# Kernel tuning notes

Hardware: AMD Instinct MI355X
Metric: run time of the kernel (lower is better)

## Reference

```python
import jax, jax.numpy as jnp
import numpy as np

B, T, D_IN, H, L, D_OUT = 32, 512, 512, 1024, 2, 512


def _init(key, shape, fan_in):
    bound = 1.0 / np.sqrt(fan_in)
    return jax.random.uniform(key, shape, jnp.float32, -bound, bound)


def setup_inputs() -> dict:
    key = jax.random.key(0)
    ks = jax.random.split(key, 16)
    inp = {"x": jax.random.normal(ks[0], (B, T, D_IN), jnp.float32)}
    # layer 0: input D_IN -> H ; layer 1: input H -> H
    inp["W_ih0"] = _init(ks[1], (3 * H, D_IN), H)
    inp["W_hh0"] = _init(ks[2], (3 * H, H), H)
    inp["b_ih0"] = _init(ks[3], (3 * H,), H)
    inp["b_hh0"] = _init(ks[4], (3 * H,), H)
    inp["W_ih1"] = _init(ks[5], (3 * H, H), H)
    inp["W_hh1"] = _init(ks[6], (3 * H, H), H)
    inp["b_ih1"] = _init(ks[7], (3 * H,), H)
    inp["b_hh1"] = _init(ks[8], (3 * H,), H)
    inp["W_fc"] = _init(ks[9], (D_OUT, H), H)
    inp["b_fc"] = _init(ks[10], (D_OUT,), H)
    return inp


def _gru_layer(x_tbd, Wih, Whh, bih, bhh):
    """x_tbd: [T, B, D]. Returns output sequence [T, B, H].
    PyTorch GRUCell gating:
      r = sigmoid(xr + hr); z = sigmoid(xz + hz)
      n = tanh(xn + r * hn); h' = (1 - z) * n + z * h
    """
    # precompute input projections for all timesteps: [T, B, 3H]
    x_proj = jnp.einsum('tbd,gd->tbg', x_tbd, Wih) + bih
    h0 = jnp.zeros((x_tbd.shape[1], Whh.shape[1]), x_tbd.dtype)

    def step(h, xp):
        hp = h @ Whh.T + bhh  # [B, 3H]
        xr, xz, xn = jnp.split(xp, 3, axis=-1)
        hr, hz, hn = jnp.split(hp, 3, axis=-1)
        r = jax.nn.sigmoid(xr + hr)
        z = jax.nn.sigmoid(xz + hz)
        n = jnp.tanh(xn + r * hn)
        h_new = (1.0 - z) * n + z * h
        return h_new, h_new

    _, out_seq = jax.lax.scan(step, h0, x_proj)
    return out_seq  # [T, B, H]


def reference(x, W_ih0, W_hh0, b_ih0, b_hh0, W_ih1, W_hh1, b_ih1, b_hh1, W_fc, b_fc):
    x_tbd = jnp.transpose(x, (1, 0, 2))  # [T, B, D_IN]
    h1_seq = _gru_layer(x_tbd, W_ih0, W_hh0, b_ih0, b_hh0)   # [T, B, H]
    h2_seq = _gru_layer(h1_seq, W_ih1, W_hh1, b_ih1, b_hh1)  # [T, B, H]
    last = h2_seq[-1]  # outs[-1].squeeze() -> [B, H]
    return last @ W_fc.T + b_fc  # [B, D_OUT]
```

## Files before the change

kernel.cpp:

```cpp
#include <hip/hip_runtime.h>

typedef unsigned short ushort;
typedef __attribute__((ext_vector_type(8))) short short8;
typedef __attribute__((ext_vector_type(4))) float f32x4;
typedef __attribute__((ext_vector_type(4))) unsigned short us4;
typedef __attribute__((ext_vector_type(4))) unsigned int u32x4;

#define BB 32
#define TT 512
#define DIN 512
#define HH 1024
#define CHUNK 128
#define SENT 0xFFFFFFFFu

__device__ __forceinline__ ushort f2b(float f) {
  unsigned u = __builtin_bit_cast(unsigned, f);
  unsigned r = (u + 0x7fffu + ((u >> 16) & 1u)) >> 16;
  return (ushort)r;
}

#define MFMA16(a, b, c) __builtin_amdgcn_mfma_f32_16x16x32_bf16(a, b, c, 0, 0, 0)

__device__ __forceinline__ void AS(unsigned* p, unsigned v) {
  __hip_atomic_store(p, v, __ATOMIC_RELAXED, __HIP_MEMORY_SCOPE_AGENT);
}

__device__ __forceinline__ bool fok(const u32x4& v) {
  return v[0] != SENT && v[1] != SENT && v[2] != SENT && v[3] != SENT;
}

__device__ __forceinline__ void poll8(const ushort* b, short8* f) {
  u32x4 t0, t1, t2, t3, t4, t5, t6, t7;
  while (true) {
    asm volatile(
        "global_load_dwordx4 %0, %8, off sc0 sc1\n\t"
        "global_load_dwordx4 %1, %9, off sc0 sc1\n\t"
        "global_load_dwordx4 %2, %10, off sc0 sc1\n\t"
        "global_load_dwordx4 %3, %11, off sc0 sc1\n\t"
        "global_load_dwordx4 %4, %12, off sc0 sc1\n\t"
        "global_load_dwordx4 %5, %13, off sc0 sc1\n\t"
        "global_load_dwordx4 %6, %14, off sc0 sc1\n\t"
        "global_load_dwordx4 %7, %15, off sc0 sc1\n\t"
        "s_waitcnt vmcnt(0)"
        : "=&v"(t0), "=&v"(t1), "=&v"(t2), "=&v"(t3),
          "=&v"(t4), "=&v"(t5), "=&v"(t6), "=&v"(t7)
        : "v"(b), "v"(b + 32), "v"(b + 64), "v"(b + 96),
          "v"(b + 128), "v"(b + 160), "v"(b + 192), "v"(b + 224)
        : "memory");
    bool ok = fok(t0) && fok(t1) && fok(t2) && fok(t3) &&
              fok(t4) && fok(t5) && fok(t6) && fok(t7);
    if (__all((int)ok)) break;
    __builtin_amdgcn_s_sleep(1);
  }
  f[0] = __builtin_bit_cast(short8, t0); f[1] = __builtin_bit_cast(short8, t1);
  f[2] = __builtin_bit_cast(short8, t2); f[3] = __builtin_bit_cast(short8, t3);
  f[4] = __builtin_bit_cast(short8, t4); f[5] = __builtin_bit_cast(short8, t5);
  f[6] = __builtin_bit_cast(short8, t6); f[7] = __builtin_bit_cast(short8, t7);
}

__device__ __forceinline__ void poll4(const ushort* b, short8* f) {
  u32x4 t0, t1, t2, t3;
  while (true) {
    asm volatile(
        "global_load_dwordx4 %0, %4, off sc0 sc1\n\t"
        "global_load_dwordx4 %1, %5, off sc0 sc1\n\t"
        "global_load_dwordx4 %2, %6, off sc0 sc1\n\t"
        "global_load_dwordx4 %3, %7, off sc0 sc1\n\t"
        "s_waitcnt vmcnt(0)"
        : "=&v"(t0), "=&v"(t1), "=&v"(t2), "=&v"(t3)
        : "v"(b), "v"(b + 32), "v"(b + 64), "v"(b + 96)
        : "memory");
    bool ok = fok(t0) && fok(t1) && fok(t2) && fok(t3);
    if (__all((int)ok)) break;
    __builtin_amdgcn_s_sleep(1);
  }
  f[0] = __builtin_bit_cast(short8, t0); f[1] = __builtin_bit_cast(short8, t1);
  f[2] = __builtin_bit_cast(short8, t2); f[3] = __builtin_bit_cast(short8, t3);
}

__global__ __launch_bounds__(256) void init_k(unsigned int* h1s, unsigned int* h2s) {
  int i = blockIdx.x * 256 + threadIdx.x;
  if (i < 16384) h1s[i] = 0u;
  else h2s[i - 16384] = 0u;
}

__global__ __launch_bounds__(256) void refill_k(u32x4* a, u32x4* b) {
  size_t i = (size_t)blockIdx.x * 256 + threadIdx.x;
  u32x4 s = {SENT, SENT, SENT, SENT};
  a[i] = s;
  b[i] = s;
}

__global__ __launch_bounds__(256) void cast_k(const float* __restrict__ in,
                                              ushort* __restrict__ out, int n4) {
  int i = blockIdx.x * 256 + threadIdx.x;
  if (i < n4) {
    float4 v = ((const float4*)in)[i];
    us4 o;
    o.x = f2b(v.x); o.y = f2b(v.y); o.z = f2b(v.z); o.w = f2b(v.w);
    ((us4*)out)[i] = o;
  }
}

__global__ __launch_bounds__(256) void gemm_bt(const float* __restrict__ A32,
                                               const ushort* __restrict__ B,
                                               float* __restrict__ C,
                                               int N, int K, int tOff) {
  __shared__ __align__(16) ushort As[128 * 72];
  __shared__ __align__(16) ushort Bs[128 * 72];
  const int tid = threadIdx.x;
  const int lane = tid & 63, wave = tid >> 6;
  const int wm = wave >> 1, wn = wave & 1;
  const int bm = blockIdx.y << 7, bn = blockIdx.x << 7;

  const int srow = tid >> 3;
  const int sdst = (tid & 7) << 3;
  size_t aoff[4], boff[4];
#pragma unroll
  for (int i = 0; i < 4; ++i) {
    int m = bm + srow + (i << 5);
    aoff[i] = ((size_t)(m & 31) * TT + tOff + (m >> 5)) * (size_t)K;
    boff[i] = (size_t)(bn + srow + (i << 5)) * K;
  }

  const int fr = lane & 15, fq = lane >> 4;
  int aofl[4], bofl[4];
#pragma unroll
  for (int m = 0; m < 4; ++m) {
    aofl[m] = ((wm << 6) + (m << 4) + fr) * 72 + (fq << 3);
    bofl[m] = ((wn << 6) + (m << 4) + fr) * 72 + (fq << 3);
  }

  f32x4 acc[4][4] = {};
  for (int k0 = 0; k0 < K; k0 += 64) {
#pragma unroll
    for (int i = 0; i < 4; ++i) {
      int row = srow + (i << 5);
      float4 v0 = *(const float4*)&A32[aoff[i] + k0 + sdst];
      float4 v1 = *(const float4*)&A32[aoff[i] + k0 + sdst + 4];
      us4 lo, hi;
      lo.x = f2b(v0.x); lo.y = f2b(v0.y); lo.z = f2b(v0.z); lo.w = f2b(v0.w);
      hi.x = f2b(v1.x); hi.y = f2b(v1.y); hi.z = f2b(v1.z); hi.w = f2b(v1.w);
      *(us4*)&As[row * 72 + sdst] = lo;
      *(us4*)&As[row * 72 + sdst + 4] = hi;
      *(short8*)&Bs[row * 72 + sdst] = *(const short8*)&B[boff[i] + k0 + sdst];
    }
    __syncthreads();
#pragma unroll
    for (int kk = 0; kk < 2; ++kk) {
      short8 af[4], bf[4];
#pragma unroll
      for (int m = 0; m < 4; ++m) af[m] = *(const short8*)&As[aofl[m] + kk * 32];
#pragma unroll
      for (int n = 0; n < 4; ++n) bf[n] = *(const short8*)&Bs[bofl[n] + kk * 32];
#pragma unroll
      for (int m = 0; m < 4; ++m)
#pragma unroll
        for (int n = 0; n < 4; ++n)
          acc[m][n] = MFMA16(af[m], bf[n], acc[m][n]);
    }
    __syncthreads();
  }
#pragma unroll
  for (int m = 0; m < 4; ++m) {
    int row0 = bm + (wm << 6) + (m << 4) + (fq << 2);
#pragma unroll
    for (int n = 0; n < 4; ++n) {
      int col = bn + (wn << 6) + (n << 4) + fr;
#pragma unroll
      for (int r = 0; r < 4; ++r)
        C[(size_t)(row0 + r) * N + col] = acc[m][n][r];
    }
  }
}

__global__ __launch_bounds__(512, 1) void gru_fused(
    const ushort* __restrict__ wh0, const ushort* __restrict__ wh1,
    const ushort* __restrict__ wi1,
    const float* __restrict__ bih0, const float* __restrict__ bhh0,
    const float* __restrict__ bih1, const float* __restrict__ bhh1,
    const float* __restrict__ xp,
    ushort* __restrict__ h1, ushort* __restrict__ h2,
    float* __restrict__ hs0, float* __restrict__ hs1,
    int t0, int nSteps) {
  __shared__ float P[8][24][64];
  const int tid = threadIdx.x;
  const int wv = tid >> 6, lane = tid & 63;
  const int fr = lane & 15, fq = lane >> 4;
  const int layer = blockIdx.x >> 6;
  const int c0 = (blockIdx.x & 63) << 4;
  const int c = c0 + fr;
  const int cpair = c0 + (fr & ~1);

  if (layer == 0) {
    const int K0 = wv << 7;
    short8 wf[3][4];
#pragma unroll
    for (int g = 0; g < 3; ++g)
#pragma unroll
      for (int j = 0; j < 4; ++j)
        wf[g][j] = *(const short8*)&wh0[(size_t)(g * HH + c) * HH + K0 + j * 32 + fq * 8];

    float bhr = 0, bhz = 0, bhn = 0, bir = 0, biz = 0, bin_ = 0;
    float hl[4] = {};
    if (wv < 2) {
      bhr = bhh0[c]; bhz = bhh0[HH + c]; bhn = bhh0[2 * HH + c];
      bir = bih0[c]; biz = bih0[HH + c]; bin_ = bih0[2 * HH + c];
      if (t0 > 0)
#pragma unroll
        for (int r = 0; r < 4; ++r) hl[r] = hs0[(wv * 16 + (fq << 2) + r) * HH + c];
    }

    for (int i = 0; i < nSteps; ++i) {
      float xr[4], xz[4], xn[4];
      if (wv < 2) {
        const float* xpt = xp + (size_t)i * (BB * 3 * HH);
#pragma unroll
        for (int r = 0; r < 4; ++r) {
          const float* p = xpt + (size_t)(wv * 16 + (fq << 2) + r) * (3 * HH) + c;
          xr[r] = p[0]; xz[r] = p[HH]; xn[r] = p[2 * HH];
        }
      }
      const ushort* sb = h1 + (size_t)i * (BB * HH);
      short8 a0[4], a1[4];
      poll4(sb + fr * HH + K0 + fq * 8, a0);
      poll4(sb + (fr + 16) * HH + K0 + fq * 8, a1);
      f32x4 acc[2][3] = {};
#pragma unroll
      for (int j = 0; j < 4; ++j) {
        acc[0][0] = MFMA16(a0[j], wf[0][j], acc[0][0]);
        acc[0][1] = MFMA16(a0[j], wf[1][j], acc[0][1]);
        acc[0][2] = MFMA16(a0[j], wf[2][j], acc[0][2]);
        acc[1][0] = MFMA16(a1[j], wf[0][j], acc[1][0]);
        acc[1][1] = MFMA16(a1[j], wf[1][j], acc[1][1]);
        acc[1][2] = MFMA16(a1[j], wf[2][j], acc[1][2]);
      }
#pragma unroll
      for (int mt = 0; mt < 2; ++mt)
#pragma unroll
        for (int g = 0; g < 3; ++g)
#pragma unroll
          for (int r = 0; r < 4; ++r)
            P[wv][mt * 12 + g * 4 + r][lane] = acc[mt][g][r];
      __syncthreads();

      if (wv < 2) {
        float s[3][4];
#pragma unroll
        for (int g = 0; g < 3; ++g)
#pragma unroll
          for (int r = 0; r < 4; ++r) {
            int e = wv * 12 + g * 4 + r;
            float v = 0.f;
#pragma unroll
            for (int w = 0; w < 8; ++w) v += P[w][e][lane];
            s[g][r] = v;
          }
        ushort* hw = h1 + (size_t)(i + 1) * (BB * HH);
        const bool last = (i == nSteps - 1);
#pragma unroll
        for (int r = 0; r < 4; ++r) {
          float rv = 1.f / (1.f + __expf(-(xr[r] + bir + s[0][r] + bhr)));
          float zv = 1.f / (1.f + __expf(-(xz[r] + biz + s[1][r] + bhz)));
          float nv = tanhf(xn[r] + bin_ + rv * (s[2][r] + bhn));
          float h = (1.f - zv) * nv + zv * hl[r];
          hl[r] = h;
          unsigned me = f2b(h);
          unsigned nb = (unsigned)__shfl_xor((int)me, 1);
          unsigned word = me | (nb << 16);
          int b = wv * 16 + (fq << 2) + r;
          if ((lane & 1) == 0)
            AS((unsigned*)(hw + (size_t)b * HH + cpair), word);
          if (last) {
            hs0[b * HH + c] = h;
            if ((lane & 1) == 0)
              *(unsigned*)(h1 + (size_t)b * HH + cpair) = word;
          }
        }
      }
      __syncthreads();
    }
  } else {
    const int K0 = (wv & 3) << 8;
    const ushort* Wm = (wv < 4) ? wh1 : wi1;
    short8 wf[3][8];
#pragma unroll
    for (int g = 0; g < 3; ++g)
#pragma unroll
      for (int j = 0; j < 8; ++j)
        wf[g][j] = *(const short8*)&Wm[(size_t)(g * HH + c) * HH + K0 + j * 32 + fq * 8];

    float bhr = 0, bhz = 0, bhn = 0, bir = 0, biz = 0, bin_ = 0;
    float hl[4] = {};
    if (wv < 2) {
      bhr = bhh1[c]; bhz = bhh1[HH + c]; bhn = bhh1[2 * HH + c];
      bir = bih1[c]; biz = bih1[HH + c]; bin_ = bih1[2 * HH + c];
      if (t0 > 0)
#pragma unroll
        for (int r = 0; r < 4; ++r) hl[r] = hs1[(wv * 16 + (fq << 2) + r) * HH + c];
    }

    for (int i = 0; i < nSteps; ++i) {
      const ushort* sb = (wv < 4) ? h2 + (size_t)i * (BB * HH)
                                  : h1 + (size_t)(i + 1) * (BB * HH);
      short8 a0[8], a1[8];
      poll8(sb + fr * HH + K0 + fq * 8, a0);
      f32x4 acc[2][3] = {};
#pragma unroll
      for (int j = 0; j < 8; ++j) {
        acc[0][0] = MFMA16(a0[j], wf[0][j], acc[0][0]);
        acc[0][1] = MFMA16(a0[j], wf[1][j], acc[0][1]);
        acc[0][2] = MFMA16(a0[j], wf[2][j], acc[0][2]);
      }
      poll8(sb + (fr + 16) * HH + K0 + fq * 8, a1);
#pragma unroll
      for (int j = 0; j < 8; ++j) {
        acc[1][0] = MFMA16(a1[j], wf[0][j], acc[1][0]);
        acc[1][1] = MFMA16(a1[j], wf[1][j], acc[1][1]);
        acc[1][2] = MFMA16(a1[j], wf[2][j], acc[1][2]);
      }
#pragma unroll
      for (int mt = 0; mt < 2; ++mt)
#pragma unroll
        for (int g = 0; g < 3; ++g)
#pragma unroll
          for (int r = 0; r < 4; ++r)
            P[wv][mt * 12 + g * 4 + r][lane] = acc[mt][g][r];
      __syncthreads();

      if (wv < 2) {
        float sh[3][4], sx[3][4];
#pragma unroll
        for (int g = 0; g < 3; ++g)
#pragma unroll
          for (int r = 0; r < 4; ++r) {
            int e = wv * 12 + g * 4 + r;
            float vh = 0.f, vx = 0.f;
#pragma unroll
            for (int w = 0; w < 4; ++w) vh += P[w][e][lane];
#pragma unroll
            for (int w = 4; w < 8; ++w) vx += P[w][e][lane];
            sh[g][r] = vh; sx[g][r] = vx;
          }
        ushort* hw = h2 + (size_t)(i + 1) * (BB * HH);
        const bool last = (i == nSteps - 1);
#pragma unroll
        for (int r = 0; r < 4; ++r) {
          float rv = 1.f / (1.f + __expf(-(sx[0][r] + bir + sh[0][r] + bhr)));
          float zv = 1.f / (1.f + __expf(-(sx[1][r] + biz + sh[1][r] + bhz)));
          float nv = tanhf(sx[2][r] + bin_ + rv * (sh[2][r] + bhn));
          float h = (1.f - zv) * nv + zv * hl[r];
          hl[r] = h;
          unsigned me = f2b(h);
          unsigned nb = (unsigned)__shfl_xor((int)me, 1);
          unsigned word = me | (nb << 16);
          int b = wv * 16 + (fq << 2) + r;
          if (!last) {
            if ((lane & 1) == 0)
              AS((unsigned*)(hw + (size_t)b * HH + cpair), word);
          } else {
            hs1[b * HH + c] = h;
            if ((lane & 1) == 0)
              *(unsigned*)(h2 + (size_t)b * HH + cpair) = word;
          }
        }
      }
      __syncthreads();
    }
  }
}

__global__ __launch_bounds__(256) void fc_k(const float* __restrict__ h,
                                            const float* __restrict__ Wf,
                                            const float* __restrict__ bf,
                                            float* __restrict__ out) {
  int idx = blockIdx.x * 256 + threadIdx.x;
  int b = idx >> 9, o = idx & 511;
  const float4* hv = (const float4*)(h + (b << 10));
  const float4* wv = (const float4*)(Wf + (o << 10));
  float s = 0.f;
#pragma unroll 8
  for (int i = 0; i < 256; ++i) {
    float4 x = hv[i], y = wv[i];
    s += x.x * y.x + x.y * y.y + x.z * y.z + x.w * y.w;
  }
  out[idx] = s + bf[o];
}

extern "C" void kernel_launch(void* const* d_in, const int* in_sizes, int n_in,
                              void* d_out, int out_size, void* d_ws, size_t ws_size,
                              hipStream_t stream) {
  const float* x    = (const float*)d_in[0];
  const float* Wih0 = (const float*)d_in[1];
  const float* Whh0 = (const float*)d_in[2];
  const float* bih0 = (const float*)d_in[3];
  const float* bhh0 = (const float*)d_in[4];
  const float* Wih1 = (const float*)d_in[5];
  const float* Whh1 = (const float*)d_in[6];
  const float* bih1 = (const float*)d_in[7];
  const float* bhh1 = (const float*)d_in[8];
  const float* Wfc  = (const float*)d_in[9];
  const float* bfc  = (const float*)d_in[10];
  float* out = (float*)d_out;

  char* w = (char*)d_ws;
  ushort* wi0b = (ushort*)(w);
  ushort* wh0b = (ushort*)(w + 3145728);
  ushort* wi1b = (ushort*)(w + 9437184);
  ushort* wh1b = (ushort*)(w + 15728640);
  float*  xp   = (float*)(w + 22020096);
  ushort* h1   = (ushort*)(w + 72351744);
  ushort* h2   = (ushort*)(w + 80805888);
  float*  hs0  = (float*)(w + 89260032);
  float*  hs1  = (float*)(w + 89391104);

  init_k<<<128, 256, 0, stream>>>((unsigned int*)h1, (unsigned int*)h2);

  cast_k<<<1536, 256, 0, stream>>>(Wih0, wi0b, (3 * HH * DIN) / 4);
  cast_k<<<3072, 256, 0, stream>>>(Whh0, wh0b, (3 * HH * HH) / 4);
  cast_k<<<3072, 256, 0, stream>>>(Wih1, wi1b, (3 * HH * HH) / 4);
  cast_k<<<3072, 256, 0, stream>>>(Whh1, wh1b, (3 * HH * HH) / 4);

  for (int ch = 0; ch < 4; ++ch) {
    const int t0 = ch * CHUNK;
    gemm_bt<<<dim3(24, 32), 256, 0, stream>>>(x, wi0b, xp, 3 * HH, DIN, t0);
    refill_k<<<2048, 256, 0, stream>>>((u32x4*)(h1 + BB * HH), (u32x4*)(h2 + BB * HH));
    gru_fused<<<128, 512, 0, stream>>>(wh0b, wh1b, wi1b, bih0, bhh0, bih1, bhh1,
                                       xp, h1, h2, hs0, hs1, t0, CHUNK);
  }

  fc_k<<<64, 256, 0, stream>>>(hs1, Wfc, bfc, out);
}
```

Baseline: 3.931 ms.

## Replace sentinel polling with per-block step flags and transposed hidden-state layout

```diff
diff --git a/kernel.cpp b/kernel.cpp
--- a/kernel.cpp
+++ b/kernel.cpp
@@ -1,17 +1,16 @@
 #include <hip/hip_runtime.h>
 
 typedef unsigned short ushort;
+typedef unsigned long long ull;
 typedef __attribute__((ext_vector_type(8))) short short8;
 typedef __attribute__((ext_vector_type(4))) float f32x4;
 typedef __attribute__((ext_vector_type(4))) unsigned short us4;
-typedef __attribute__((ext_vector_type(4))) unsigned int u32x4;
 
 #define BB 32
 #define TT 512
 #define DIN 512
 #define HH 1024
 #define CHUNK 128
-#define SENT 0xFFFFFFFFu
 
 __device__ __forceinline__ ushort f2b(float f) {
   unsigned u = __builtin_bit_cast(unsigned, f);
@@ -20,75 +19,17 @@
 }
 
 #define MFMA16(a, b, c) __builtin_amdgcn_mfma_f32_16x16x32_bf16(a, b, c, 0, 0, 0)
-
-__device__ __forceinline__ void AS(unsigned* p, unsigned v) {
-  __hip_atomic_store(p, v, __ATOMIC_RELAXED, __HIP_MEMORY_SCOPE_AGENT);
-}
-
-__device__ __forceinline__ bool fok(const u32x4& v) {
-  return v[0] != SENT && v[1] != SENT && v[2] != SENT && v[3] != SENT;
-}
-
-__device__ __forceinline__ void poll8(const ushort* b, short8* f) {
-  u32x4 t0, t1, t2, t3, t4, t5, t6, t7;
-  while (true) {
-    asm volatile(
-        "global_load_dwordx4 %0, %8, off sc0 sc1\n\t"
-        "global_load_dwordx4 %1, %9, off sc0 sc1\n\t"
-        "global_load_dwordx4 %2, %10, off sc0 sc1\n\t"
-        "global_load_dwordx4 %3, %11, off sc0 sc1\n\t"
-        "global_load_dwordx4 %4, %12, off sc0 sc1\n\t"
-        "global_load_dwordx4 %5, %13, off sc0 sc1\n\t"
-        "global_load_dwordx4 %6, %14, off sc0 sc1\n\t"
-        "global_load_dwordx4 %7, %15, off sc0 sc1\n\t"
-        "s_waitcnt vmcnt(0)"
-        : "=&v"(t0), "=&v"(t1), "=&v"(t2), "=&v"(t3),
-          "=&v"(t4), "=&v"(t5), "=&v"(t6), "=&v"(t7)
-        : "v"(b), "v"(b + 32), "v"(b + 64), "v"(b + 96),
-          "v"(b + 128), "v"(b + 160), "v"(b + 192), "v"(b + 224)
-        : "memory");
-    bool ok = fok(t0) && fok(t1) && fok(t2) && fok(t3) &&
-              fok(t4) && fok(t5) && fok(t6) && fok(t7);
-    if (__all((int)ok)) break;
-    __builtin_amdgcn_s_sleep(1);
-  }
-  f[0] = __builtin_bit_cast(short8, t0); f[1] = __builtin_bit_cast(short8, t1);
-  f[2] = __builtin_bit_cast(short8, t2); f[3] = __builtin_bit_cast(short8, t3);
-  f[4] = __builtin_bit_cast(short8, t4); f[5] = __builtin_bit_cast(short8, t5);
-  f[6] = __builtin_bit_cast(short8, t6); f[7] = __builtin_bit_cast(short8, t7);
-}
-
-__device__ __forceinline__ void poll4(const ushort* b, short8* f) {
-  u32x4 t0, t1, t2, t3;
-  while (true) {
-    asm volatile(
-        "global_load_dwordx4 %0, %4, off sc0 sc1\n\t"
-        "global_load_dwordx4 %1, %5, off sc0 sc1\n\t"
-        "global_load_dwordx4 %2, %6, off sc0 sc1\n\t"
-        "global_load_dwordx4 %3, %7, off sc0 sc1\n\t"
-        "s_waitcnt vmcnt(0)"
-        : "=&v"(t0), "=&v"(t1), "=&v"(t2), "=&v"(t3)
-        : "v"(b), "v"(b + 32), "v"(b + 64), "v"(b + 96)
-        : "memory");
-    bool ok = fok(t0) && fok(t1) && fok(t2) && fok(t3);
-    if (__all((int)ok)) break;
-    __builtin_amdgcn_s_sleep(1);
-  }
-  f[0] = __builtin_bit_cast(short8, t0); f[1] = __builtin_bit_cast(short8, t1);
-  f[2] = __builtin_bit_cast(short8, t2); f[3] = __builtin_bit_cast(short8, t3);
-}
-
-__global__ __launch_bounds__(256) void init_k(unsigned int* h1s, unsigned int* h2s) {
+#define AL(p) __hip_atomic_load((p), __ATOMIC_RELAXED, __HIP_MEMORY_SCOPE_AGENT)
+
+union U8 { unsigned u[4]; short8 s; };
+
+__global__ __launch_bounds__(256) void init_k(unsigned int* h1s, unsigned int* h2s,
+                                              int* f0, int* f1) {
   int i = blockIdx.x * 256 + threadIdx.x;
   if (i < 16384) h1s[i] = 0u;
   else h2s[i - 16384] = 0u;
-}
-
-__global__ __launch_bounds__(256) void refill_k(u32x4* a, u32x4* b) {
-  size_t i = (size_t)blockIdx.x * 256 + threadIdx.x;
-  u32x4 s = {SENT, SENT, SENT, SENT};
-  a[i] = s;
-  b[i] = s;
+  if (i < 128) f0[i] = 0;
+  else if (i < 256) f1[i - 128] = 0;
 }
 
 __global__ __launch_bounds__(256) void cast_k(const float* __restrict__ in,
@@ -174,23 +115,24 @@
   }
 }
 
-__global__ __launch_bounds__(512, 1) void gru_fused(
+__global__ __launch_bounds__(512, 2) void gru_fused(
     const ushort* __restrict__ wh0, const ushort* __restrict__ wh1,
     const ushort* __restrict__ wi1,
     const float* __restrict__ bih0, const float* __restrict__ bhh0,
     const float* __restrict__ bih1, const float* __restrict__ bhh1,
     const float* __restrict__ xp,
-    ushort* __restrict__ h1, ushort* __restrict__ h2,
+    ushort* __restrict__ h1t, ushort* __restrict__ h2t,
     float* __restrict__ hs0, float* __restrict__ hs1,
+    int* __restrict__ f0, int* __restrict__ f1,
     int t0, int nSteps) {
   __shared__ float P[8][24][64];
   const int tid = threadIdx.x;
   const int wv = tid >> 6, lane = tid & 63;
   const int fr = lane & 15, fq = lane >> 4;
   const int layer = blockIdx.x >> 6;
-  const int c0 = (blockIdx.x & 63) << 4;
+  const int wg = blockIdx.x & 63;
+  const int c0 = wg << 4;
   const int c = c0 + fr;
-  const int cpair = c0 + (fr & ~1);
 
   if (layer == 0) {
     const int K0 = wv << 7;
@@ -212,6 +154,7 @@
     }
 
     for (int i = 0; i < nSteps; ++i) {
+      const int t = t0 + i;
       float xr[4], xz[4], xn[4];
       if (wv < 2) {
         const float* xpt = xp + (size_t)i * (BB * 3 * HH);
@@ -221,10 +164,29 @@
           xr[r] = p[0]; xz[r] = p[HH]; xn[r] = p[2 * HH];
         }
       }
-      const ushort* sb = h1 + (size_t)i * (BB * HH);
+      asm volatile("" ::: "memory");
+      {
+        int v0, v1;
+        do {
+          v0 = AL(f0 + lane); v1 = AL(f0 + 64 + lane);
+          if (v0 < t || v1 < t) __builtin_amdgcn_s_sleep(1);
+        } while (__any(v0 < t || v1 < t));
+      }
+      asm volatile("" ::: "memory");
+
+      const ushort* sb = h1t + (size_t)i * 32768;
       short8 a0[4], a1[4];
-      poll4(sb + fr * HH + K0 + fq * 8, a0);
-      poll4(sb + (fr + 16) * HH + K0 + fq * 8, a1);
+#pragma unroll
+      for (int j = 0; j < 4; ++j) {
+        const ushort* p = sb + ((K0 + j * 32 + fq * 8) << 5) + fr;
+        U8 x0, x1;
+#pragma unroll
+        for (int q = 0; q < 4; ++q) {
+          x0.u[q] = (unsigned)p[(2 * q) * 32] | ((unsigned)p[(2 * q + 1) * 32] << 16);
+          x1.u[q] = (unsigned)p[(2 * q) * 32 + 16] | ((unsigned)p[(2 * q + 1) * 32 + 16] << 16);
+        }
+        a0[j] = x0.s; a1[j] = x1.s;
+      }
       f32x4 acc[2][3] = {};
 #pragma unroll
       for (int j = 0; j < 4; ++j) {
@@ -256,27 +218,30 @@
             for (int w = 0; w < 8; ++w) v += P[w][e][lane];
             s[g][r] = v;
           }
-        ushort* hw = h1 + (size_t)(i + 1) * (BB * HH);
-        const bool last = (i == nSteps - 1);
+        float hv[4];
 #pragma unroll
         for (int r = 0; r < 4; ++r) {
           float rv = 1.f / (1.f + __expf(-(xr[r] + bir + s[0][r] + bhr)));
           float zv = 1.f / (1.f + __expf(-(xz[r] + biz + s[1][r] + bhz)));
           float nv = tanhf(xn[r] + bin_ + rv * (s[2][r] + bhn));
-          float h = (1.f - zv) * nv + zv * hl[r];
-          hl[r] = h;
-          unsigned me = f2b(h);
-          unsigned nb = (unsigned)__shfl_xor((int)me, 1);
-          unsigned word = me | (nb << 16);
-          int b = wv * 16 + (fq << 2) + r;
-          if ((lane & 1) == 0)
-            AS((unsigned*)(hw + (size_t)b * HH + cpair), word);
-          if (last) {
-            hs0[b * HH + c] = h;
-            if ((lane & 1) == 0)
-              *(unsigned*)(h1 + (size_t)b * HH + cpair) = word;
-          }
-        }
+          hv[r] = (1.f - zv) * nv + zv * hl[r];
+          hl[r] = hv[r];
+        }
+        ull word = (ull)((unsigned)f2b(hv[0]) | ((unsigned)f2b(hv[1]) << 16)) |
+                   ((ull)((unsigned)f2b(hv[2]) | ((unsigned)f2b(hv[3]) << 16)) << 32);
+        const int toff = (c0 + fr) * 32 + wv * 16 + fq * 4;
+        __hip_atomic_store((ull*)(h1t + (size_t)(i + 1) * 32768 + toff), word,
+                           __ATOMIC_RELAXED, __HIP_MEMORY_SCOPE_AGENT);
+        if (i == nSteps - 1) {
+          *(ull*)(h1t + toff) = word;
+#pragma unroll
+          for (int r = 0; r < 4; ++r)
+            hs0[(wv * 16 + (fq << 2) + r) * HH + c] = hv[r];
+        }
+        asm volatile("s_waitcnt vmcnt(0)" ::: "memory");
+        if (lane == 0)
+          __hip_atomic_store(f0 + wv * 64 + wg, t + 1,
+                             __ATOMIC_RELAXED, __HIP_MEMORY_SCOPE_AGENT);
       }
       __syncthreads();
     }
@@ -301,23 +266,56 @@
     }
 
     for (int i = 0; i < nSteps; ++i) {
-      const ushort* sb = (wv < 4) ? h2 + (size_t)i * (BB * HH)
-                                  : h1 + (size_t)(i + 1) * (BB * HH);
-      short8 a0[8], a1[8];
-      poll8(sb + fr * HH + K0 + fq * 8, a0);
+      const int t = t0 + i;
+      {
+        int ok;
+        do {
+          int a = AL(f1 + lane), b = AL(f1 + 64 + lane);
+          int d = AL(f0 + lane), e = AL(f0 + 64 + lane);
+          ok = (a >= t) && (b >= t) && (d >= t + 1) && (e >= t + 1);
+          if (!ok) __builtin_amdgcn_s_sleep(1);
+        } while (__any(!ok));
+      }
+      asm volatile("" ::: "memory");
+
+      const ushort* sb = (wv < 4) ? h2t + (size_t)i * 32768
+                                  : h1t + (size_t)(i + 1) * 32768;
       f32x4 acc[2][3] = {};
-#pragma unroll
-      for (int j = 0; j < 8; ++j) {
-        acc[0][0] = MFMA16(a0[j], wf[0][j], acc[0][0]);
-        acc[0][1] = MFMA16(a0[j], wf[1][j], acc[0][1]);
-        acc[0][2] = MFMA16(a0[j], wf[2][j], acc[0][2]);
-      }
-      poll8(sb + (fr + 16) * HH + K0 + fq * 8, a1);
-#pragma unroll
-      for (int j = 0; j < 8; ++j) {
-        acc[1][0] = MFMA16(a1[j], wf[0][j], acc[1][0]);
-        acc[1][1] = MFMA16(a1[j], wf[1][j], acc[1][1]);
-        acc[1][2] = MFMA16(a1[j], wf[2][j], acc[1][2]);
+      {
+        short8 a0[8];
+#pragma unroll
+        for (int j = 0; j < 8; ++j) {
+          const ushort* p = sb + ((K0 + j * 32 + fq * 8) << 5) + fr;
+          U8 x0;
+#pragma unroll
+          for (int q = 0; q < 4; ++q)
+            x0.u[q] = (unsigned)p[(2 * q) * 32] | ((unsigned)p[(2 * q + 1) * 32] << 16);
+          a0[j] = x0.s;
+        }
+#pragma unroll
+        for (int j = 0; j < 8; ++j) {
+          acc[0][0] = MFMA16(a0[j], wf[0][j], acc[0][0]);
+          acc[0][1] = MFMA16(a0[j], wf[1][j], acc[0][1]);
+          acc[0][2] = MFMA16(a0[j], wf[2][j], acc[0][2]);
+        }
+      }
+      {
+        short8 a1[8];
+#pragma unroll
+        for (int j = 0; j < 8; ++j) {
+          const ushort* p = sb + ((K0 + j * 32 + fq * 8) << 5) + fr + 16;
+          U8 x1;
+#pragma unroll
+          for (int q = 0; q < 4; ++q)
+            x1.u[q] = (unsigned)p[(2 * q) * 32] | ((unsigned)p[(2 * q + 1) * 32] << 16);
+          a1[j] = x1.s;
+        }
+#pragma unroll
+        for (int j = 0; j < 8; ++j) {
+          acc[1][0] = MFMA16(a1[j], wf[0][j], acc[1][0]);
+          acc[1][1] = MFMA16(a1[j], wf[1][j], acc[1][1]);
+          acc[1][2] = MFMA16(a1[j], wf[2][j], acc[1][2]);
+        }
       }
 #pragma unroll
       for (int mt = 0; mt < 2; ++mt)
@@ -342,28 +340,30 @@
             for (int w = 4; w < 8; ++w) vx += P[w][e][lane];
             sh[g][r] = vh; sx[g][r] = vx;
           }
-        ushort* hw = h2 + (size_t)(i + 1) * (BB * HH);
-        const bool last = (i == nSteps - 1);
+        float hv[4];
 #pragma unroll
         for (int r = 0; r < 4; ++r) {
           float rv = 1.f / (1.f + __expf(-(sx[0][r] + bir + sh[0][r] + bhr)));
           float zv = 1.f / (1.f + __expf(-(sx[1][r] + biz + sh[1][r] + bhz)));
           float nv = tanhf(sx[2][r] + bin_ + rv * (sh[2][r] + bhn));
-          float h = (1.f - zv) * nv + zv * hl[r];
-          hl[r] = h;
-          unsigned me = f2b(h);
-          unsigned nb = (unsigned)__shfl_xor((int)me, 1);
-          unsigned word = me | (nb << 16);
-          int b = wv * 16 + (fq << 2) + r;
-          if (!last) {
-            if ((lane & 1) == 0)
-              AS((unsigned*)(hw + (size_t)b * HH + cpair), word);
-          } else {
-            hs1[b * HH + c] = h;
-            if ((lane & 1) == 0)
-              *(unsigned*)(h2 + (size_t)b * HH + cpair) = word;
-          }
-        }
+          hv[r] = (1.f - zv) * nv + zv * hl[r];
+          hl[r] = hv[r];
+        }
+        ull word = (ull)((unsigned)f2b(hv[0]) | ((unsigned)f2b(hv[1]) << 16)) |
+                   ((ull)((unsigned)f2b(hv[2]) | ((unsigned)f2b(hv[3]) << 16)) << 32);
+        const int toff = (c0 + fr) * 32 + wv * 16 + fq * 4;
+        __hip_atomic_store((ull*)(h2t + (size_t)(i + 1) * 32768 + toff), word,
+                           __ATOMIC_RELAXED, __HIP_MEMORY_SCOPE_AGENT);
+        if (i == nSteps - 1) {
+          *(ull*)(h2t + toff) = word;
+#pragma unroll
+          for (int r = 0; r < 4; ++r)
+            hs1[(wv * 16 + (fq << 2) + r) * HH + c] = hv[r];
+        }
+        asm volatile("s_waitcnt vmcnt(0)" ::: "memory");
+        if (lane == 0)
+          __hip_atomic_store(f1 + wv * 64 + wg, t + 1,
+                             __ATOMIC_RELAXED, __HIP_MEMORY_SCOPE_AGENT);
       }
       __syncthreads();
     }
@@ -409,12 +409,14 @@
   ushort* wi1b = (ushort*)(w + 9437184);
   ushort* wh1b = (ushort*)(w + 15728640);
   float*  xp   = (float*)(w + 22020096);
-  ushort* h1   = (ushort*)(w + 72351744);
-  ushort* h2   = (ushort*)(w + 80805888);
+  ushort* h1t  = (ushort*)(w + 72351744);
+  ushort* h2t  = (ushort*)(w + 80805888);
   float*  hs0  = (float*)(w + 89260032);
   float*  hs1  = (float*)(w + 89391104);
-
-  init_k<<<128, 256, 0, stream>>>((unsigned int*)h1, (unsigned int*)h2);
+  int*    f0   = (int*)(w + 89522176);
+  int*    f1   = (int*)(w + 89522688);
+
+  init_k<<<128, 256, 0, stream>>>((unsigned int*)h1t, (unsigned int*)h2t, f0, f1);
 
   cast_k<<<1536, 256, 0, stream>>>(Wih0, wi0b, (3 * HH * DIN) / 4);
   cast_k<<<3072, 256, 0, stream>>>(Whh0, wh0b, (3 * HH * HH) / 4);
@@ -424,9 +426,8 @@
   for (int ch = 0; ch < 4; ++ch) {
     const int t0 = ch * CHUNK;
     gemm_bt<<<dim3(24, 32), 256, 0, stream>>>(x, wi0b, xp, 3 * HH, DIN, t0);
-    refill_k<<<2048, 256, 0, stream>>>((u32x4*)(h1 + BB * HH), (u32x4*)(h2 + BB * HH));
     gru_fused<<<128, 512, 0, stream>>>(wh0b, wh1b, wi1b, bih0, bhh0, bih1, bhh1,
-                                       xp, h1, h2, hs0, hs1, t0, CHUNK);
+                                       xp, h1t, h2t, hs0, hs1, f0, f1, t0, CHUNK);
   }
 
   fc_k<<<64, 256, 0, stream>>>(hs1, Wfc, bfc, out);
```

Result: no change. 3.958 ms (+0.7%).
